# Kernel optimization log

Measured on AMD Instinct MI355X. Metric: run time of the kernel, lower is better.

Reference implementation:

```python
import jax, jax.numpy as jnp
import numpy as np

MD_S = 1
MD_R = 16
EVAL_STEPS = 7
INV_T = 100.0
EPS = 1e-6

B, C, S = 16, 512, 4096  # batch, channels, flattened spatial


def setup_inputs() -> dict:
    key = jax.random.key(0)
    k1, k2 = jax.random.split(key)
    x = jax.random.uniform(k1, (B, C, S), dtype=jnp.float32)  # non-negative input for NMF
    bases = jax.random.uniform(k2, (B * MD_S, S, MD_R), dtype=jnp.float32)
    # F.normalize(bases, dim=1)
    bases = bases / (jnp.linalg.norm(bases, axis=1, keepdims=True) + 1e-12)
    return {"x": x, "bases": bases}


def _nmf_step(xm, bases, coef):
    # xm: (BS, D, N), bases: (BS, D, R), coef: (BS, N, R)
    # multiplicative update for coef
    num = jnp.einsum('bdn,bdr->bnr', xm, bases)
    den = jnp.einsum('bnr,brs->bns', coef, jnp.einsum('bdr,bds->brs', bases, bases))
    coef = coef * num / (den + EPS)
    # multiplicative update for bases
    num = jnp.einsum('bdn,bnr->bdr', xm, coef)
    den = jnp.einsum('bdr,brs->bds', bases, jnp.einsum('bnr,bns->brs', coef, coef))
    bases = bases * num / (den + EPS)
    return bases, coef


def _local_inference(xm, bases):
    # coef init: softmax(inv_t * x^T bases)
    coef = jax.nn.softmax(INV_T * jnp.einsum('bdn,bdr->bnr', xm, bases), axis=-1)

    def body(carry, _):
        b, c = _nmf_step(xm, carry[0], carry[1])
        return (b, c), None

    (bases, coef), _ = jax.lax.scan(body, (bases, coef), None, length=EVAL_STEPS)
    return bases, coef


def reference(x, bases):
    Bb, Cc, Ss = x.shape
    D = Ss
    N = Cc // MD_S
    xm = x.reshape(Bb * MD_S, N, D).transpose(0, 2, 1)  # (BS, D, N)

    bases_i, coef_i = jax.lax.stop_gradient(_local_inference(xm, bases))

    # compute_coef (differentiable in the original module)
    num = jnp.einsum('bdn,bdr->bnr', xm, bases_i)
    den = jnp.einsum('bnr,brs->bns', coef_i, jnp.einsum('bdr,bds->brs', bases_i, bases_i))
    coef = coef_i * num / (den + EPS)

    # x_rec = bases @ coef^T -> (BS, D, N) -> transpose -> (B, C, S)
    out = jnp.einsum('bdr,bnr->bdn', bases_i, coef)
    out = out.transpose(0, 2, 1).reshape(Bb, Cc, Ss)
    return out
```

## Files before the change

kernel.cpp:

```cpp
#include <hip/hip_runtime.h>

#define EPS 1e-6f

template <int CTRL>
__device__ __forceinline__ float dpp_add(float v) {
  int moved = __builtin_amdgcn_update_dpp(0, __float_as_int(v), CTRL, 0xF, 0xF, false);
  return v + __int_as_float(moved);
}

__global__ __launch_bounds__(512) void kernelA(
    const float* __restrict__ x, const float* __restrict__ bases,
    float* __restrict__ P, float* __restrict__ coef,
    float* __restrict__ CtC, int do_softmax)
{
  __shared__ __align__(16) float lb[20480];
  const int tid = threadIdx.x;
  if (blockIdx.x < 16 && tid < 256) CtC[blockIdx.x * 256 + tid] = 0.0f;
  const int b = blockIdx.x >> 4;
  const int grp = blockIdx.x & 15;
  const int w = tid >> 6;
  const int lane = tid & 63;
  const int h = w >> 2;
  const int rg = w & 3;
  const int n0 = grp * 32 + rg * 8;
  const float* __restrict__ xp = x + ((size_t)(b * 512 + n0)) * 4096 + h * 2048;
  const float4* __restrict__ srcf4 = (const float4*)(bases + ((size_t)b) * 4096 * 16);

  float acc[8][16];
#pragma unroll
  for (int i = 0; i < 8; ++i)
#pragma unroll
    for (int r = 0; r < 16; ++r) acc[i][r] = 0.0f;

  for (int c = 0; c < 4; ++c) {
#pragma unroll
    for (int k = 0; k < 8; ++k) {
      int idx = k * 512 + tid;
      int buf = idx >> 11;
      int rem = idx & 2047;
      int dl = rem >> 2, q = rem & 3;
      int cg = c + buf * 4;
      *(float4*)(&lb[buf * 10240 + dl * 20 + q * 4]) = srcf4[(cg * 512 + dl) * 4 + q];
    }
    __syncthreads();
    const float* __restrict__ lbh = lb + h * 10240;
    const float* __restrict__ xpc = xp + c * 512;
#pragma unroll
    for (int j = 0; j < 8; ++j) {
      const int dl = j * 64 + lane;
      float xv[8];
#pragma unroll
      for (int i = 0; i < 8; ++i) xv[i] = xpc[(size_t)i * 4096 + dl];
      const float* row = &lbh[dl * 20];
#pragma unroll
      for (int q = 0; q < 4; ++q) {
        float4 bv = *(const float4*)(row + q * 4);
#pragma unroll
        for (int i = 0; i < 8; ++i) {
          acc[i][q * 4 + 0] = fmaf(xv[i], bv.x, acc[i][q * 4 + 0]);
          acc[i][q * 4 + 1] = fmaf(xv[i], bv.y, acc[i][q * 4 + 1]);
          acc[i][q * 4 + 2] = fmaf(xv[i], bv.z, acc[i][q * 4 + 2]);
          acc[i][q * 4 + 3] = fmaf(xv[i], bv.w, acc[i][q * 4 + 3]);
        }
      }
    }
    __syncthreads();
  }

#pragma unroll
  for (int i = 0; i < 8; ++i)
#pragma unroll
    for (int r = 0; r < 16; ++r) {
      float v = acc[i][r];
      v = dpp_add<0x121>(v);
      v = dpp_add<0x122>(v);
      v = dpp_add<0x124>(v);
      v = dpp_add<0x128>(v);
      v += __shfl_xor(v, 16, 64);
      v += __shfl_xor(v, 32, 64);
      acc[i][r] = v;
    }

  if (lane == 0) {
#pragma unroll
    for (int i = 0; i < 8; ++i)
#pragma unroll
      for (int r = 0; r < 16; ++r) lb[(h * 4 + rg) * 128 + i * 16 + r] = acc[i][r];
  }
  __syncthreads();
  {
    const int row = tid >> 4;
    const int r = tid & 15;
    const int prg = row >> 3, pi = row & 7;
    float p = lb[(prg)*128 + pi * 16 + r] + lb[(4 + prg) * 128 + pi * 16 + r];
    P[((size_t)(b * 512 + grp * 32 + row)) * 16 + r] = p;
    if (do_softmax) {
      lb[1024 + tid] = p;
      __syncthreads();
      if (tid < 32) {
        const float* pf = &lb[1024 + tid * 16];
        float m = pf[0];
#pragma unroll
        for (int rr = 1; rr < 16; ++rr) m = fmaxf(m, pf[rr]);
        float e[16];
        float s = 0.0f;
#pragma unroll
        for (int rr = 0; rr < 16; ++rr) { e[rr] = __expf(100.0f * (pf[rr] - m)); s += e[rr]; }
        float inv = 1.0f / s;
        float* __restrict__ crow = coef + ((size_t)(b * 512 + grp * 32 + tid)) * 16;
#pragma unroll
        for (int rr = 0; rr < 16; ++rr) crow[rr] = e[rr] * inv;
      }
    }
  }
}

__global__ __launch_bounds__(256) void kernelGram(
    const float* __restrict__ M, float* __restrict__ out, int L)
{
  __shared__ __align__(16) float sm[256 * 20];
  __shared__ __align__(16) float part[4 * 272];
  const int tid = threadIdx.x;
  const int b = blockIdx.y;
  const int sl = blockIdx.x;
  const float4* __restrict__ src = (const float4*)(M + ((size_t)b * L + (size_t)sl * 256) * 16);
#pragma unroll
  for (int k = 0; k < 4; ++k) {
    int idx = k * 256 + tid;
    int row = idx >> 2, q = idx & 3;
    *(float4*)(&sm[row * 20 + q * 4]) = src[idx];
  }
  __syncthreads();
  const int rq = tid & 3;
  const int s = (tid >> 2) & 15;
  const int g = tid >> 6;
  float a0 = 0.f, a1 = 0.f, a2 = 0.f, a3 = 0.f;
#pragma unroll 4
  for (int l = g * 64; l < g * 64 + 64; ++l) {
    float4 bv = *(const float4*)(&sm[l * 20 + rq * 4]);
    float cs = sm[l * 20 + s];
    a0 = fmaf(cs, bv.x, a0);
    a1 = fmaf(cs, bv.y, a1);
    a2 = fmaf(cs, bv.z, a2);
    a3 = fmaf(cs, bv.w, a3);
  }
  *(float4*)(&part[g * 272 + s * 16 + rq * 4]) = make_float4(a0, a1, a2, a3);
  __syncthreads();
  float v = part[0 * 272 + tid] + part[1 * 272 + tid] + part[2 * 272 + tid] + part[3 * 272 + tid];
  atomicAdd(out + b * 256 + tid, v);
}

__global__ __launch_bounds__(256) void kernelCU(
    float* __restrict__ coef, const float* __restrict__ P,
    const float* __restrict__ BtBr, float* __restrict__ BtBz,
    float* __restrict__ CtCadd)
{
  __shared__ __align__(16) float sm[256 * 20 + 4 * 272];
  const int tid = threadIdx.x;
  BtBz[blockIdx.x * 128 + (tid & 127)] = 0.0f;
  const int b = blockIdx.x >> 1;
  const int n = ((blockIdx.x & 1) << 8) + tid;
  float* __restrict__ crow = coef + ((size_t)(b * 512 + n)) * 16;
  const float* __restrict__ prow = P + ((size_t)(b * 512 + n)) * 16;
  const float* __restrict__ btb = BtBr + b * 256;
  float cv[16], den[16];
#pragma unroll
  for (int r = 0; r < 16; ++r) cv[r] = crow[r];
#pragma unroll
  for (int r = 0; r < 16; ++r) den[r] = 0.f;
#pragma unroll
  for (int s2 = 0; s2 < 16; ++s2) {
    const float bs = cv[s2];
#pragma unroll
    for (int r = 0; r < 16; ++r) den[r] = fmaf(bs, btb[s2 * 16 + r], den[r]);
  }
#pragma unroll
  for (int r = 0; r < 16; ++r) {
    float cn = cv[r] * prow[r] / (den[r] + EPS);
    crow[r] = cn;
    sm[tid * 20 + r] = cn;
  }
  __syncthreads();
  const int rq = tid & 3;
  const int s = (tid >> 2) & 15;
  const int g = tid >> 6;
  float a0 = 0.f, a1 = 0.f, a2 = 0.f, a3 = 0.f;
#pragma unroll 4
  for (int l = g * 64; l < g * 64 + 64; ++l) {
    float4 bv = *(const float4*)(&sm[l * 20 + rq * 4]);
    float cs = sm[l * 20 + s];
    a0 = fmaf(cs, bv.x, a0);
    a1 = fmaf(cs, bv.y, a1);
    a2 = fmaf(cs, bv.z, a2);
    a3 = fmaf(cs, bv.w, a3);
  }
  float* part = sm + 5120;
  *(float4*)(&part[g * 272 + s * 16 + rq * 4]) = make_float4(a0, a1, a2, a3);
  __syncthreads();
  float v = part[0 * 272 + tid] + part[1 * 272 + tid] + part[2 * 272 + tid] + part[3 * 272 + tid];
  atomicAdd(CtCadd + b * 256 + tid, v);
}

__global__ __launch_bounds__(256) void kernelBacc(
    const float* __restrict__ x, const float* __restrict__ coef,
    float* __restrict__ qpart)
{
  const int tid = threadIdx.x;
  const int dt = blockIdx.x, ns = blockIdx.y, b = blockIdx.z;
  const int d = dt * 256 + tid;
  const float* __restrict__ xp = x + ((size_t)(b * 512 + ns * 128)) * 4096 + d;
  const float* __restrict__ cp = coef + ((size_t)(b * 512 + ns * 128)) * 16;
  float acc[16];
#pragma unroll
  for (int r = 0; r < 16; ++r) acc[r] = 0.f;
#pragma unroll 4
  for (int n = 0; n < 128; ++n) {
    const float xv = xp[(size_t)n * 4096];
    const float* __restrict__ crow = cp + n * 16;
#pragma unroll
    for (int r = 0; r < 16; ++r) acc[r] = fmaf(xv, crow[r], acc[r]);
  }
  float* __restrict__ qp = qpart + (((size_t)(ns * 16 + b)) * 4096 + d) * 16;
#pragma unroll
  for (int q = 0; q < 4; ++q)
    *(float4*)(qp + q * 4) = make_float4(acc[q * 4], acc[q * 4 + 1], acc[q * 4 + 2], acc[q * 4 + 3]);
}

__global__ __launch_bounds__(256) void kernelBfin(
    const float* __restrict__ qpart, float* __restrict__ bases,
    const float* __restrict__ CtC, float* __restrict__ BtBadd)
{
  __shared__ __align__(16) float sm[256 * 20 + 4 * 272];
  const int tid = threadIdx.x;
  const int dt = blockIdx.x, b = blockIdx.y;
  const int d = dt * 256 + tid;
  float acc[16];
#pragma unroll
  for (int r = 0; r < 16; ++r) acc[r] = 0.f;
#pragma unroll
  for (int ns = 0; ns < 4; ++ns) {
    const float* __restrict__ qp = qpart + (((size_t)(ns * 16 + b)) * 4096 + d) * 16;
#pragma unroll
    for (int q = 0; q < 4; ++q) {
      float4 v = *(const float4*)(qp + q * 4);
      acc[q * 4 + 0] += v.x; acc[q * 4 + 1] += v.y; acc[q * 4 + 2] += v.z; acc[q * 4 + 3] += v.w;
    }
  }
  float* __restrict__ brow = bases + ((size_t)(b * 4096 + d)) * 16;
  float bv[16];
#pragma unroll
  for (int r = 0; r < 16; ++r) bv[r] = brow[r];
  const float* __restrict__ ctc = CtC + b * 256;
  float den[16];
#pragma unroll
  for (int r = 0; r < 16; ++r) den[r] = 0.f;
#pragma unroll
  for (int s2 = 0; s2 < 16; ++s2) {
    const float bs = bv[s2];
#pragma unroll
    for (int r = 0; r < 16; ++r) den[r] = fmaf(bs, ctc[s2 * 16 + r], den[r]);
  }
#pragma unroll
  for (int r = 0; r < 16; ++r) {
    float bn = bv[r] * acc[r] / (den[r] + EPS);
    brow[r] = bn;
    sm[tid * 20 + r] = bn;
  }
  __syncthreads();
  const int rq = tid & 3;
  const int s = (tid >> 2) & 15;
  const int g = tid >> 6;
  float a0 = 0.f, a1 = 0.f, a2 = 0.f, a3 = 0.f;
#pragma unroll 4
  for (int l = g * 64; l < g * 64 + 64; ++l) {
    float4 bq = *(const float4*)(&sm[l * 20 + rq * 4]);
    float cs = sm[l * 20 + s];
    a0 = fmaf(cs, bq.x, a0);
    a1 = fmaf(cs, bq.y, a1);
    a2 = fmaf(cs, bq.z, a2);
    a3 = fmaf(cs, bq.w, a3);
  }
  float* part = sm + 5120;
  *(float4*)(&part[g * 272 + s * 16 + rq * 4]) = make_float4(a0, a1, a2, a3);
  __syncthreads();
  float v = part[0 * 272 + tid] + part[1 * 272 + tid] + part[2 * 272 + tid] + part[3 * 272 + tid];
  atomicAdd(BtBadd + b * 256 + tid, v);
}

__global__ __launch_bounds__(256) void kernelOut(
    const float* __restrict__ bases, const float* __restrict__ coef,
    float* __restrict__ out)
{
  const int tid = threadIdx.x;
  const int dt = blockIdx.x, ns = blockIdx.y, b = blockIdx.z;
  const int d0 = dt * 1024 + tid * 4;
  float bv[4][16];
#pragma unroll
  for (int k = 0; k < 4; ++k) {
    const float* __restrict__ brow = bases + ((size_t)(b * 4096 + d0 + k)) * 16;
#pragma unroll
    for (int r = 0; r < 16; ++r) bv[k][r] = brow[r];
  }
  const float* __restrict__ cp = coef + ((size_t)(b * 512 + ns * 32)) * 16;
  float* __restrict__ op = out + ((size_t)(b * 512 + ns * 32)) * 4096 + d0;
#pragma unroll 4
  for (int n = 0; n < 32; ++n) {
    const float* __restrict__ crow = cp + n * 16;
    float v[4];
#pragma unroll
    for (int k = 0; k < 4; ++k) {
      float s = 0.f;
#pragma unroll
      for (int r = 0; r < 16; ++r) s = fmaf(bv[k][r], crow[r], s);
      v[k] = s;
    }
    *(float4*)(op + (size_t)n * 4096) = make_float4(v[0], v[1], v[2], v[3]);
  }
}

extern "C" void kernel_launch(void* const* d_in, const int* in_sizes, int n_in,
                              void* d_out, int out_size, void* d_ws, size_t ws_size,
                              hipStream_t stream) {
  const float* x = (const float*)d_in[0];
  const float* bases_in = (const float*)d_in[1];
  float* out = (float*)d_out;
  float* ws = (float*)d_ws;

  float* bases = ws;
  float* coef  = bases + 1048576;
  float* P     = coef + 131072;
  float* btb0  = P + 131072;
  float* btb1  = btb0 + 4096;
  float* ctc   = btb1 + 4096;
  float* qpart = ctc + 4096;
  float* btb[2] = {btb0, btb1};

  hipMemsetAsync(btb0, 0, 4096 * sizeof(float), stream);
  hipMemcpyAsync(bases, bases_in, 1048576 * sizeof(float),
                 hipMemcpyDeviceToDevice, stream);

  kernelA<<<256, 512, 0, stream>>>(x, bases, P, coef, ctc, 1);
  kernelGram<<<dim3(16, 16), 256, 0, stream>>>(bases, btb0, 4096);

  for (int t = 0; t < 7; ++t) {
    if (t > 0) kernelA<<<256, 512, 0, stream>>>(x, bases, P, coef, ctc, 0);
    kernelCU<<<32, 256, 0, stream>>>(coef, P, btb[t & 1], btb[(t + 1) & 1], ctc);
    kernelBacc<<<dim3(16, 4, 16), 256, 0, stream>>>(x, coef, qpart);
    kernelBfin<<<dim3(16, 16), 256, 0, stream>>>(qpart, bases, ctc, btb[(t + 1) & 1]);
  }

  kernelA<<<256, 512, 0, stream>>>(x, bases, P, coef, ctc, 0);
  kernelCU<<<32, 256, 0, stream>>>(coef, P, btb[1], btb[0], ctc);
  kernelOut<<<dim3(4, 16, 16), 256, 0, stream>>>(bases, coef, out);
}
```

Baseline: 1.101 ms.

## Split kernelA over D halves into separate blocks with partial outputs

kernelA now launches twice as many blocks, each handling one half of the spatial D dimension. Each block now holds 8×8 accumulators per thread and splits the 16 rank columns across its two wave halves, which cuts register pressure and the shared-memory footprint and raises occupancy (launch_bounds 512,4). The two D-half partial results are written to a partial buffer and summed later in kernelCU. The initial softmax moves into a separate small kernelSM. The trade-off is extra global traffic for the partials, each x element is now read by two waves instead of one, and there is one extra launch.

Result: faster. 1.019 ms (-7.4%).

```diff
diff --git a/kernel.cpp b/kernel.cpp
--- a/kernel.cpp
+++ b/kernel.cpp
@@ -8,60 +8,58 @@
   return v + __int_as_float(moved);
 }
 
-__global__ __launch_bounds__(512) void kernelA(
+__global__ __launch_bounds__(512, 4) void kernelA(
     const float* __restrict__ x, const float* __restrict__ bases,
-    float* __restrict__ P, float* __restrict__ coef,
-    float* __restrict__ CtC, int do_softmax)
-{
-  __shared__ __align__(16) float lb[20480];
-  const int tid = threadIdx.x;
-  if (blockIdx.x < 16 && tid < 256) CtC[blockIdx.x * 256 + tid] = 0.0f;
-  const int b = blockIdx.x >> 4;
-  const int grp = blockIdx.x & 15;
+    float* __restrict__ Ppart, float* __restrict__ CtC)
+{
+  __shared__ __align__(16) float lb[512 * 20];
+  const int tid = threadIdx.x;
+  const int grp = blockIdx.x;
+  const int b = blockIdx.y;
+  const int h = blockIdx.z;
+  if (h == 0 && grp == 0 && tid < 256) CtC[b * 256 + tid] = 0.0f;
   const int w = tid >> 6;
   const int lane = tid & 63;
-  const int h = w >> 2;
   const int rg = w & 3;
+  const int rh = w >> 2;
   const int n0 = grp * 32 + rg * 8;
   const float* __restrict__ xp = x + ((size_t)(b * 512 + n0)) * 4096 + h * 2048;
-  const float4* __restrict__ srcf4 = (const float4*)(bases + ((size_t)b) * 4096 * 16);
-
-  float acc[8][16];
+  const float4* __restrict__ srcf4 =
+      (const float4*)(bases + ((size_t)(b * 4096 + h * 2048)) * 16);
+
+  float acc[8][8];
 #pragma unroll
   for (int i = 0; i < 8; ++i)
 #pragma unroll
-    for (int r = 0; r < 16; ++r) acc[i][r] = 0.0f;
+    for (int r = 0; r < 8; ++r) acc[i][r] = 0.0f;
 
   for (int c = 0; c < 4; ++c) {
 #pragma unroll
-    for (int k = 0; k < 8; ++k) {
+    for (int k = 0; k < 4; ++k) {
       int idx = k * 512 + tid;
-      int buf = idx >> 11;
-      int rem = idx & 2047;
-      int dl = rem >> 2, q = rem & 3;
-      int cg = c + buf * 4;
-      *(float4*)(&lb[buf * 10240 + dl * 20 + q * 4]) = srcf4[(cg * 512 + dl) * 4 + q];
+      int dl = idx >> 2, q = idx & 3;
+      *(float4*)(&lb[dl * 20 + q * 4]) = srcf4[(c * 512 + dl) * 4 + q];
     }
     __syncthreads();
-    const float* __restrict__ lbh = lb + h * 10240;
     const float* __restrict__ xpc = xp + c * 512;
 #pragma unroll
     for (int j = 0; j < 8; ++j) {
       const int dl = j * 64 + lane;
+      float4 b0 = *(const float4*)(&lb[dl * 20 + rh * 8]);
+      float4 b1 = *(const float4*)(&lb[dl * 20 + rh * 8 + 4]);
       float xv[8];
 #pragma unroll
       for (int i = 0; i < 8; ++i) xv[i] = xpc[(size_t)i * 4096 + dl];
-      const float* row = &lbh[dl * 20];
-#pragma unroll
-      for (int q = 0; q < 4; ++q) {
-        float4 bv = *(const float4*)(row + q * 4);
-#pragma unroll
-        for (int i = 0; i < 8; ++i) {
-          acc[i][q * 4 + 0] = fmaf(xv[i], bv.x, acc[i][q * 4 + 0]);
-          acc[i][q * 4 + 1] = fmaf(xv[i], bv.y, acc[i][q * 4 + 1]);
-          acc[i][q * 4 + 2] = fmaf(xv[i], bv.z, acc[i][q * 4 + 2]);
-          acc[i][q * 4 + 3] = fmaf(xv[i], bv.w, acc[i][q * 4 + 3]);
-        }
+#pragma unroll
+      for (int i = 0; i < 8; ++i) {
+        acc[i][0] = fmaf(xv[i], b0.x, acc[i][0]);
+        acc[i][1] = fmaf(xv[i], b0.y, acc[i][1]);
+        acc[i][2] = fmaf(xv[i], b0.z, acc[i][2]);
+        acc[i][3] = fmaf(xv[i], b0.w, acc[i][3]);
+        acc[i][4] = fmaf(xv[i], b1.x, acc[i][4]);
+        acc[i][5] = fmaf(xv[i], b1.y, acc[i][5]);
+        acc[i][6] = fmaf(xv[i], b1.z, acc[i][6]);
+        acc[i][7] = fmaf(xv[i], b1.w, acc[i][7]);
       }
     }
     __syncthreads();
@@ -70,7 +68,7 @@
 #pragma unroll
   for (int i = 0; i < 8; ++i)
 #pragma unroll
-    for (int r = 0; r < 16; ++r) {
+    for (int r = 0; r < 8; ++r) {
       float v = acc[i][r];
       v = dpp_add<0x121>(v);
       v = dpp_add<0x122>(v);
@@ -82,37 +80,37 @@
     }
 
   if (lane == 0) {
-#pragma unroll
-    for (int i = 0; i < 8; ++i)
-#pragma unroll
-      for (int r = 0; r < 16; ++r) lb[(h * 4 + rg) * 128 + i * 16 + r] = acc[i][r];
-  }
-  __syncthreads();
-  {
-    const int row = tid >> 4;
-    const int r = tid & 15;
-    const int prg = row >> 3, pi = row & 7;
-    float p = lb[(prg)*128 + pi * 16 + r] + lb[(4 + prg) * 128 + pi * 16 + r];
-    P[((size_t)(b * 512 + grp * 32 + row)) * 16 + r] = p;
-    if (do_softmax) {
-      lb[1024 + tid] = p;
-      __syncthreads();
-      if (tid < 32) {
-        const float* pf = &lb[1024 + tid * 16];
-        float m = pf[0];
-#pragma unroll
-        for (int rr = 1; rr < 16; ++rr) m = fmaxf(m, pf[rr]);
-        float e[16];
-        float s = 0.0f;
-#pragma unroll
-        for (int rr = 0; rr < 16; ++rr) { e[rr] = __expf(100.0f * (pf[rr] - m)); s += e[rr]; }
-        float inv = 1.0f / s;
-        float* __restrict__ crow = coef + ((size_t)(b * 512 + grp * 32 + tid)) * 16;
-#pragma unroll
-        for (int rr = 0; rr < 16; ++rr) crow[rr] = e[rr] * inv;
-      }
-    }
-  }
+    float* __restrict__ pp =
+        Ppart + (((size_t)(h * 16 + b)) * 512 + n0) * 16 + rh * 8;
+#pragma unroll
+    for (int i = 0; i < 8; ++i) {
+      *(float4*)(pp + i * 16) = make_float4(acc[i][0], acc[i][1], acc[i][2], acc[i][3]);
+      *(float4*)(pp + i * 16 + 4) = make_float4(acc[i][4], acc[i][5], acc[i][6], acc[i][7]);
+    }
+  }
+}
+
+__global__ __launch_bounds__(256) void kernelSM(
+    const float* __restrict__ Ppart, float* __restrict__ coef)
+{
+  const int gid = blockIdx.x * 256 + threadIdx.x;
+  const int b = gid >> 9, n = gid & 511;
+  const float* __restrict__ p0 = Ppart + (((size_t)b) * 512 + n) * 16;
+  const float* __restrict__ p1 = Ppart + (((size_t)(16 + b)) * 512 + n) * 16;
+  float p[16];
+#pragma unroll
+  for (int r = 0; r < 16; ++r) p[r] = p0[r] + p1[r];
+  float m = p[0];
+#pragma unroll
+  for (int r = 1; r < 16; ++r) m = fmaxf(m, p[r]);
+  float e[16];
+  float s = 0.0f;
+#pragma unroll
+  for (int r = 0; r < 16; ++r) { e[r] = __expf(100.0f * (p[r] - m)); s += e[r]; }
+  float inv = 1.0f / s;
+  float* __restrict__ crow = coef + (((size_t)b) * 512 + n) * 16;
+#pragma unroll
+  for (int r = 0; r < 16; ++r) crow[r] = e[r] * inv;
 }
 
 __global__ __launch_bounds__(256) void kernelGram(
@@ -151,7 +149,7 @@
 }
 
 __global__ __launch_bounds__(256) void kernelCU(
-    float* __restrict__ coef, const float* __restrict__ P,
+    float* __restrict__ coef, const float* __restrict__ Ppart,
     const float* __restrict__ BtBr, float* __restrict__ BtBz,
     float* __restrict__ CtCadd)
 {
@@ -161,7 +159,8 @@
   const int b = blockIdx.x >> 1;
   const int n = ((blockIdx.x & 1) << 8) + tid;
   float* __restrict__ crow = coef + ((size_t)(b * 512 + n)) * 16;
-  const float* __restrict__ prow = P + ((size_t)(b * 512 + n)) * 16;
+  const float* __restrict__ p0 = Ppart + (((size_t)b) * 512 + n) * 16;
+  const float* __restrict__ p1 = Ppart + (((size_t)(16 + b)) * 512 + n) * 16;
   const float* __restrict__ btb = BtBr + b * 256;
   float cv[16], den[16];
 #pragma unroll
@@ -176,7 +175,7 @@
   }
 #pragma unroll
   for (int r = 0; r < 16; ++r) {
-    float cn = cv[r] * prow[r] / (den[r] + EPS);
+    float cn = cv[r] * (p0[r] + p1[r]) / (den[r] + EPS);
     crow[r] = cn;
     sm[tid * 20 + r] = cn;
   }
@@ -328,8 +327,8 @@
 
   float* bases = ws;
   float* coef  = bases + 1048576;
-  float* P     = coef + 131072;
-  float* btb0  = P + 131072;
+  float* Ppart = coef + 131072;
+  float* btb0  = Ppart + 262144;
   float* btb1  = btb0 + 4096;
   float* ctc   = btb1 + 4096;
   float* qpart = ctc + 4096;
@@ -339,17 +338,18 @@
   hipMemcpyAsync(bases, bases_in, 1048576 * sizeof(float),
                  hipMemcpyDeviceToDevice, stream);
 
-  kernelA<<<256, 512, 0, stream>>>(x, bases, P, coef, ctc, 1);
+  kernelA<<<dim3(16, 16, 2), 512, 0, stream>>>(x, bases, Ppart, ctc);
+  kernelSM<<<32, 256, 0, stream>>>(Ppart, coef);
   kernelGram<<<dim3(16, 16), 256, 0, stream>>>(bases, btb0, 4096);
 
   for (int t = 0; t < 7; ++t) {
-    if (t > 0) kernelA<<<256, 512, 0, stream>>>(x, bases, P, coef, ctc, 0);
-    kernelCU<<<32, 256, 0, stream>>>(coef, P, btb[t & 1], btb[(t + 1) & 1], ctc);
+    if (t > 0) kernelA<<<dim3(16, 16, 2), 512, 0, stream>>>(x, bases, Ppart, ctc);
+    kernelCU<<<32, 256, 0, stream>>>(coef, Ppart, btb[t & 1], btb[(t + 1) & 1], ctc);
     kernelBacc<<<dim3(16, 4, 16), 256, 0, stream>>>(x, coef, qpart);
     kernelBfin<<<dim3(16, 16), 256, 0, stream>>>(qpart, bases, ctc, btb[(t + 1) & 1]);
   }
 
-  kernelA<<<256, 512, 0, stream>>>(x, bases, P, coef, ctc, 0);
-  kernelCU<<<32, 256, 0, stream>>>(coef, P, btb[1], btb[0], ctc);
+  kernelA<<<dim3(16, 16, 2), 512, 0, stream>>>(x, bases, Ppart, ctc);
+  kernelCU<<<32, 256, 0, stream>>>(coef, Ppart, btb[1], btb[0], ctc);
   kernelOut<<<dim3(4, 16, 16), 256, 0, stream>>>(bases, coef, out);
 }
```
